# Kernel tuning notes

Hardware: AMD Instinct MI355X
Metric: run time of the kernel (lower is better)

Reference implementation:

```python
import jax, jax.numpy as jnp
import numpy as np

IN_N_CH = 32
IN_BS = 1_048_576
IN_SR = 48_000
OUT_SR = 44_100
OUT_BS = -(-IN_BS * OUT_SR // IN_SR)  # ceil -> 963380


def _calc_x_and_indices(in_bs: int, out_bs: int):
    """Faithful port of InplaceLinearResampler.calc_x_and_indices +
    the 4-point neighbor indices from Inplace4pHermiteResampler.set_sample_rates."""
    scaling = (in_bs - 1) / (out_bs - 1) + 1e-12
    xf = np.arange(out_bs, dtype=np.float64) * scaling
    y0 = np.floor(xf).astype(np.int64)
    y1 = np.clip(y0 + 1, 0, in_bs - 1)
    x = np.clip(xf - y0, 0.0, 1.0)
    x[0] = 0.0
    x[-1] = np.round(x[-1])
    y_m1 = np.clip(y0 - 1, 0, in_bs - 1)
    y2 = np.clip(y1 + 1, 0, in_bs - 1)
    return (x.astype(np.float32), y_m1.astype(np.int32), y0.astype(np.int32),
            y1.astype(np.int32), y2.astype(np.int32))


def setup_inputs() -> dict:
    key = jax.random.key(0)
    y = jax.random.normal(key, (IN_N_CH, IN_BS), dtype=jnp.float32)
    x, y_m1_idx, y0_idx, y1_idx, y2_idx = _calc_x_and_indices(IN_BS, OUT_BS)
    return {
        "y": y,
        "x": jnp.asarray(x),
        "y_m1_idx": jnp.asarray(y_m1_idx),
        "y0_idx": jnp.asarray(y0_idx),
        "y1_idx": jnp.asarray(y1_idx),
        "y2_idx": jnp.asarray(y2_idx),
    }


def reference(y, x, y_m1_idx, y0_idx, y1_idx, y2_idx):
    # Gathers: [n_ch, out_bs]
    ym1 = jnp.take(y, y_m1_idx, axis=1)
    y0v = jnp.take(y, y0_idx, axis=1)
    y1v = jnp.take(y, y1_idx, axis=1)
    y2v = jnp.take(y, y2_idx, axis=1)
    # Cubic Hermite coefficients (Niemitalo 4-point, 3rd-order)
    c1 = 0.5 * (y1v - ym1)
    c2 = ym1 - 2.5 * y0v + 2.0 * y1v - 0.5 * y2v
    c3 = 0.5 * (y2v - ym1) + 1.5 * (y0v - y1v)
    # Horner evaluation: ((c3*x + c2)*x + c1)*x + c0, c0 = y0
    return ((c3 * x + c2) * x + c1) * x + y0v
```

## Files before the change

kernel.cpp:

```cpp
#include <hip/hip_runtime.h>


#define TILE 512
#define SPAN 576

typedef float vfloat2 __attribute__((ext_vector_type(2)));

template<bool INTERIOR>
__device__ __forceinline__ void run_channels(
    const float* __restrict__ y, float* __restrict__ out, float* buf,
    float4 sreg, int nchunk, int base_al, int rmax,
    int in_bs, int out_bs, int n_ch, int t, int j, float2 xv, int2 iv)
{
    for (int ch = 0; ch < n_ch; ++ch) {
        if (t < nchunk) *reinterpret_cast<float4*>(&buf[4 * t]) = sreg;
        __syncthreads();
        if (ch + 1 < n_ch) {
            const float* s2 = y + (size_t)(ch + 1) * (size_t)in_bs + base_al;
            if (t < nchunk) sreg = *reinterpret_cast<const float4*>(s2 + 4 * t);
        }
        if (j < out_bs) {
            float o0, o1;
            {
                const int r = iv.x - base_al;
                float ym1, y0v, y1v, y2v;
                if (INTERIOR) {
                    const float* p = buf + r;
                    ym1 = p[-1]; y0v = p[0]; y1v = p[1]; y2v = p[2];
                } else {
                    const int a  = max(r - 1, 0);
                    const int b1 = min(r + 1, rmax);
                    const int b2 = min(r + 2, rmax);
                    ym1 = buf[a]; y0v = buf[r]; y1v = buf[b1]; y2v = buf[b2];
                }
                const float c1 = 0.5f * (y1v - ym1);
                const float c2 = ym1 - 2.5f * y0v + 2.0f * y1v - 0.5f * y2v;
                const float c3 = 0.5f * (y2v - ym1) + 1.5f * (y0v - y1v);
                o0 = ((c3 * xv.x + c2) * xv.x + c1) * xv.x + y0v;
            }
            {
                const int r = iv.y - base_al;
                float ym1, y0v, y1v, y2v;
                if (INTERIOR) {
                    const float* p = buf + r;
                    ym1 = p[-1]; y0v = p[0]; y1v = p[1]; y2v = p[2];
                } else {
                    const int a  = max(r - 1, 0);
                    const int b1 = min(r + 1, rmax);
                    const int b2 = min(r + 2, rmax);
                    ym1 = buf[a]; y0v = buf[r]; y1v = buf[b1]; y2v = buf[b2];
                }
                const float c1 = 0.5f * (y1v - ym1);
                const float c2 = ym1 - 2.5f * y0v + 2.0f * y1v - 0.5f * y2v;
                const float c3 = 0.5f * (y2v - ym1) + 1.5f * (y0v - y1v);
                o1 = ((c3 * xv.y + c2) * xv.y + c1) * xv.y + y0v;
            }
            vfloat2 o; o.x = o0; o.y = o1;
            *reinterpret_cast<vfloat2*>(out + (size_t)ch * (size_t)out_bs + j) = o;
        }
        __syncthreads();
    }
}

__global__ __launch_bounds__(256) void hermite_lds_kernel(
    const float* __restrict__ y,
    const float* __restrict__ x,
    const int* __restrict__ y0_idx,
    float* __restrict__ out,
    int out_bs, int in_bs, int n_ch)
{
    __shared__ float buf[SPAN];
    const int t  = threadIdx.x;
    const int j0 = blockIdx.x * TILE;
    const int j  = j0 + 2 * t;

    int base = y0_idx[j0] - 1;
    if (base < 0) base = 0;
    const int base_al = base & ~3;
    const int rmax    = (in_bs - 1) - base_al;
    const int n_stage = min(SPAN, in_bs - base_al);
    const int nchunk  = n_stage >> 2;

    float2 xv = make_float2(0.f, 0.f);
    int2   iv = make_int2(base_al, base_al);
    if (j < out_bs) {
        xv = *reinterpret_cast<const float2*>(x + j);
        iv = *reinterpret_cast<const int2*>(y0_idx + j);
    }

    float4 sreg = make_float4(0.f, 0.f, 0.f, 0.f);
    if (t < nchunk)
        sreg = *reinterpret_cast<const float4*>(y + base_al + 4 * t);

    const bool interior = (base_al > 0) && (in_bs - base_al > SPAN);
    if (interior)
        run_channels<true >(y, out, buf, sreg, nchunk, base_al, rmax,
                            in_bs, out_bs, n_ch, t, j, xv, iv);
    else
        run_channels<false>(y, out, buf, sreg, nchunk, base_al, rmax,
                            in_bs, out_bs, n_ch, t, j, xv, iv);
}

extern "C" void kernel_launch(void* const* d_in, const int* in_sizes, int n_in,
                              void* d_out, int out_size, void* d_ws, size_t ws_size,
                              hipStream_t stream)
{
    const float* y   = (const float*)d_in[0];
    const float* x   = (const float*)d_in[1];
    const int*   i0  = (const int*)d_in[3];
    float*       out = (float*)d_out;

    const int out_bs = in_sizes[1];
    const int n_ch   = out_size / out_bs;
    const int in_bs  = in_sizes[0] / n_ch;

    const int grid = (out_bs + TILE - 1) / TILE;
    hermite_lds_kernel<<<grid, 256, 0, stream>>>(
        y, x, i0, out, out_bs, in_bs, n_ch);
}
```

Baseline: 50.22 us.

## Give each wave its own channels and LDS buffers, dropping block barriers

Each of the four waves in a block now owns every fourth channel and stages that channel's input span in its own double-buffered LDS region. This removes the two block-wide __syncthreads per channel. Channel data is prefetched into registers two channels ahead, and each lane now produces four output pairs per channel instead of one. The cost is more registers and a fourfold larger LDS footprint. The code also assumes the channel count is a multiple of four and relies on in-order LDS access within a wave rather than explicit barriers.

After: 54.77 us. 9.1% more time.

```diff
diff --git a/kernel.cpp b/kernel.cpp
--- a/kernel.cpp
+++ b/kernel.cpp
@@ -7,98 +7,122 @@
 typedef float vfloat2 __attribute__((ext_vector_type(2)));
 
 template<bool INTERIOR>
-__device__ __forceinline__ void run_channels(
-    const float* __restrict__ y, float* __restrict__ out, float* buf,
-    float4 sreg, int nchunk, int base_al, int rmax,
-    int in_bs, int out_bs, int n_ch, int t, int j, float2 xv, int2 iv)
+__device__ __forceinline__ float hermite1(const float* __restrict__ buf,
+                                          int r, int rmax, float xw)
 {
-    for (int ch = 0; ch < n_ch; ++ch) {
-        if (t < nchunk) *reinterpret_cast<float4*>(&buf[4 * t]) = sreg;
-        __syncthreads();
-        if (ch + 1 < n_ch) {
-            const float* s2 = y + (size_t)(ch + 1) * (size_t)in_bs + base_al;
-            if (t < nchunk) sreg = *reinterpret_cast<const float4*>(s2 + 4 * t);
+    float ym1, y0v, y1v, y2v;
+    if (INTERIOR) {
+        ym1 = buf[r - 1]; y0v = buf[r]; y1v = buf[r + 1]; y2v = buf[r + 2];
+    } else {
+        const int a  = max(r - 1, 0);
+        const int b1 = min(r + 1, rmax);
+        const int b2 = min(r + 2, rmax);
+        ym1 = buf[a]; y0v = buf[r]; y1v = buf[b1]; y2v = buf[b2];
+    }
+    const float c1 = 0.5f * (y1v - ym1);
+    const float c2 = ym1 - 2.5f * y0v + 2.0f * y1v - 0.5f * y2v;
+    const float c3 = 0.5f * (y2v - ym1) + 1.5f * (y0v - y1v);
+    return ((c3 * xw + c2) * xw + c1) * xw + y0v;
+}
+
+template<bool INTERIOR>
+__device__ __forceinline__ void channel_loop(
+    const float* __restrict__ y, float* __restrict__ out,
+    float* __restrict__ mybuf,
+    int nchunk, int base_al, int rmax, int in_bs, int out_bs, int nseg,
+    int w, int lane, int j0, const float2* xv, const int2* iv)
+{
+    const size_t chs = (size_t)in_bs;
+
+    float4 a0, a1, a2, b0, b1, b2;
+    a0 = a1 = a2 = b0 = b1 = b2 = make_float4(0.f, 0.f, 0.f, 0.f);
+    {
+        const float* p0 = y + (size_t)w * chs + base_al;
+        const float* p1 = p0 + 4 * chs;
+        if (lane < nchunk)       { a0 = *(const float4*)(p0 + 4 * lane);
+                                   b0 = *(const float4*)(p1 + 4 * lane); }
+        if (lane + 64 < nchunk)  { a1 = *(const float4*)(p0 + 4 * (lane + 64));
+                                   b1 = *(const float4*)(p1 + 4 * (lane + 64)); }
+        if (lane + 128 < nchunk) { a2 = *(const float4*)(p0 + 4 * (lane + 128));
+                                   b2 = *(const float4*)(p1 + 4 * (lane + 128)); }
+    }
+
+    #pragma unroll 2
+    for (int s = 0; s < nseg; ++s) {
+        float* bcur = mybuf + (s & 1) * SPAN;
+        if (lane < nchunk)       *(float4*)(bcur + 4 * lane)         = a0;
+        if (lane + 64 < nchunk)  *(float4*)(bcur + 4 * (lane + 64))  = a1;
+        if (lane + 128 < nchunk) *(float4*)(bcur + 4 * (lane + 128)) = a2;
+
+        float4 n0 = b0, n1 = b1, n2 = b2;
+        if (s + 2 < nseg) {
+            const float* pn = y + (size_t)(w + 4 * (s + 2)) * chs + base_al;
+            if (lane < nchunk)       b0 = *(const float4*)(pn + 4 * lane);
+            if (lane + 64 < nchunk)  b1 = *(const float4*)(pn + 4 * (lane + 64));
+            if (lane + 128 < nchunk) b2 = *(const float4*)(pn + 4 * (lane + 128));
         }
-        if (j < out_bs) {
-            float o0, o1;
-            {
-                const int r = iv.x - base_al;
-                float ym1, y0v, y1v, y2v;
-                if (INTERIOR) {
-                    const float* p = buf + r;
-                    ym1 = p[-1]; y0v = p[0]; y1v = p[1]; y2v = p[2];
-                } else {
-                    const int a  = max(r - 1, 0);
-                    const int b1 = min(r + 1, rmax);
-                    const int b2 = min(r + 2, rmax);
-                    ym1 = buf[a]; y0v = buf[r]; y1v = buf[b1]; y2v = buf[b2];
-                }
-                const float c1 = 0.5f * (y1v - ym1);
-                const float c2 = ym1 - 2.5f * y0v + 2.0f * y1v - 0.5f * y2v;
-                const float c3 = 0.5f * (y2v - ym1) + 1.5f * (y0v - y1v);
-                o0 = ((c3 * xv.x + c2) * xv.x + c1) * xv.x + y0v;
+
+        const int ch = w + 4 * s;
+        float* __restrict__ orow = out + (size_t)ch * (size_t)out_bs;
+        #pragma unroll
+        for (int it = 0; it < 4; ++it) {
+            const int j = j0 + it * 128 + lane * 2;
+            if (j < out_bs) {
+                const int r0 = iv[it].x - base_al;
+                const int r1 = iv[it].y - base_al;
+                vfloat2 o;
+                o.x = hermite1<INTERIOR>(bcur, r0, rmax, xv[it].x);
+                o.y = hermite1<INTERIOR>(bcur, r1, rmax, xv[it].y);
+                *(vfloat2*)(orow + j) = o;
             }
-            {
-                const int r = iv.y - base_al;
-                float ym1, y0v, y1v, y2v;
-                if (INTERIOR) {
-                    const float* p = buf + r;
-                    ym1 = p[-1]; y0v = p[0]; y1v = p[1]; y2v = p[2];
-                } else {
-                    const int a  = max(r - 1, 0);
-                    const int b1 = min(r + 1, rmax);
-                    const int b2 = min(r + 2, rmax);
-                    ym1 = buf[a]; y0v = buf[r]; y1v = buf[b1]; y2v = buf[b2];
-                }
-                const float c1 = 0.5f * (y1v - ym1);
-                const float c2 = ym1 - 2.5f * y0v + 2.0f * y1v - 0.5f * y2v;
-                const float c3 = 0.5f * (y2v - ym1) + 1.5f * (y0v - y1v);
-                o1 = ((c3 * xv.y + c2) * xv.y + c1) * xv.y + y0v;
-            }
-            vfloat2 o; o.x = o0; o.y = o1;
-            *reinterpret_cast<vfloat2*>(out + (size_t)ch * (size_t)out_bs + j) = o;
         }
-        __syncthreads();
+        a0 = n0; a1 = n1; a2 = n2;
     }
 }
 
-__global__ __launch_bounds__(256) void hermite_lds_kernel(
+__global__ __launch_bounds__(256) void hermite_wave_kernel(
     const float* __restrict__ y,
     const float* __restrict__ x,
     const int* __restrict__ y0_idx,
     float* __restrict__ out,
     int out_bs, int in_bs, int n_ch)
 {
-    __shared__ float buf[SPAN];
-    const int t  = threadIdx.x;
-    const int j0 = blockIdx.x * TILE;
-    const int j  = j0 + 2 * t;
+    __shared__ float buf[4][2][SPAN];
+    const int t    = threadIdx.x;
+    const int w    = t >> 6;
+    const int lane = t & 63;
+    const int j0   = blockIdx.x * TILE;
 
     int base = y0_idx[j0] - 1;
     if (base < 0) base = 0;
     const int base_al = base & ~3;
     const int rmax    = (in_bs - 1) - base_al;
-    const int n_stage = min(SPAN, in_bs - base_al);
-    const int nchunk  = n_stage >> 2;
+    const int nchunk  = min(SPAN, in_bs - base_al) >> 2;
 
-    float2 xv = make_float2(0.f, 0.f);
-    int2   iv = make_int2(base_al, base_al);
-    if (j < out_bs) {
-        xv = *reinterpret_cast<const float2*>(x + j);
-        iv = *reinterpret_cast<const int2*>(y0_idx + j);
+    float2 xv[4];
+    int2   iv[4];
+    #pragma unroll
+    for (int it = 0; it < 4; ++it) {
+        const int j = j0 + it * 128 + lane * 2;
+        if (j < out_bs) {
+            xv[it] = *(const float2*)(x + j);
+            iv[it] = *(const int2*)(y0_idx + j);
+        } else {
+            xv[it] = make_float2(0.f, 0.f);
+            iv[it] = make_int2(base_al, base_al);
+        }
     }
 
-    float4 sreg = make_float4(0.f, 0.f, 0.f, 0.f);
-    if (t < nchunk)
-        sreg = *reinterpret_cast<const float4*>(y + base_al + 4 * t);
+    const int  nseg     = n_ch >> 2;
+    const bool interior = (base_al > 0) && (in_bs - base_al > SPAN);
+    float* mybuf = &buf[w][0][0];
 
-    const bool interior = (base_al > 0) && (in_bs - base_al > SPAN);
     if (interior)
-        run_channels<true >(y, out, buf, sreg, nchunk, base_al, rmax,
-                            in_bs, out_bs, n_ch, t, j, xv, iv);
+        channel_loop<true >(y, out, mybuf, nchunk, base_al, rmax,
+                            in_bs, out_bs, nseg, w, lane, j0, xv, iv);
     else
-        run_channels<false>(y, out, buf, sreg, nchunk, base_al, rmax,
-                            in_bs, out_bs, n_ch, t, j, xv, iv);
+        channel_loop<false>(y, out, mybuf, nchunk, base_al, rmax,
+                            in_bs, out_bs, nseg, w, lane, j0, xv, iv);
 }
 
 extern "C" void kernel_launch(void* const* d_in, const int* in_sizes, int n_in,
@@ -115,6 +139,6 @@
     const int in_bs  = in_sizes[0] / n_ch;
 
     const int grid = (out_bs + TILE - 1) / TILE;
-    hermite_lds_kernel<<<grid, 256, 0, stream>>>(
+    hermite_wave_kernel<<<grid, 256, 0, stream>>>(
         y, x, i0, out, out_bs, in_bs, n_ch);
 }
```
